# Kernel tuning notes

Hardware: AMD Instinct MI355X
Metric: run time of the kernel (lower is better)

The kernel has to match this reference:

```python
import jax, jax.numpy as jnp
import numpy as np

# SPU activation from the RIAI project: x^2-0.5 for x>=0, sigmoid(-x)-1 for x<0

def _spu(x):
    return jnp.where(x >= 0, x * x - 0.5, jax.nn.sigmoid(-x) - 1.0)

def _spu_grad(x):
    return jnp.where(x <= -50.0, 0.0,
                     jnp.where(x >= 0.0, 2.0 * x, -0.5 / (jnp.cosh(x) + 1.0)))

def _spu_tangent(x0):
    a = _spu_grad(x0)
    return a, _spu(x0) - a * x0

def _tangent_param(l, u, t):
    return _spu_tangent(l * (1.0 - t) + u * t)

def _spu_shifted_over_x(x):
    normal = (x <= -1e-5) | (x > 0)
    safe_x = jnp.where(normal, x, 1.0)  # avoid 0/0 in masked-out lanes
    return jnp.where(normal, (_spu(x) + 0.5) / safe_x, -0.25)

def _binsearch_acceptable_range(l, u):
    req = _spu(u)
    bl, br = l, jnp.zeros_like(l)
    for _ in range(20):  # fixed 20 bisection steps, fully vectorized
        c = 0.5 * (bl + br)
        a, b = _spu_tangent(c)
        covers = a * u + b >= req
        bl = jnp.where(covers, c, bl)
        br = jnp.where(covers, br, c)
    return bl

def _spu_bounds(l, u, tl, tu):
    # endpoint (secant) line through (l,spu(l)) and (u,spu(u))
    yl, yu = _spu(l), _spu(u)
    ea = (yu - yl) / (u - l + 1e-8)
    eb = yl - l * ea

    negative = u <= 0
    positive = l >= 0
    crossing = ~(negative | positive)

    # negative branch (args masked: negative*l, negative*u)
    ln, un = jnp.where(negative, l, 0.0), jnp.where(negative, u, 0.0)
    na, nb = _tangent_param(ln, un, tu)
    # positive branch
    lp, up = jnp.where(positive, l, 0.0), jnp.where(positive, u, 0.0)
    pa, pb = _tangent_param(lp, up, tl)

    # crossing branch: l full, u masked (matches spu_crossing(l, crossing*u))
    uc = jnp.where(crossing, u, 0.0)
    u_end = _binsearch_acceptable_range(l, uc)
    ua, ub_ = _tangent_param(l, u_end, tu)
    not_cov = ua * uc + ub_ <= _spu(uc)
    cr_uw = jnp.where(not_cov, ea, ua)
    cr_ub = jnp.where(not_cov, eb, ub_)
    # bottom tangent (lower bound for crossing)
    den = uc - l
    threshold = -l / jnp.where(den == 0, 1.0, den)
    is_normal = tl >= threshold
    nla, nlb = _tangent_param(l, uc, tl)
    steep = _spu_shifted_over_x(l)
    safe_thr = jnp.where(threshold == 0, 1.0, threshold)
    wa = steep * (1.0 - (tl / safe_thr) ** 2)
    wb = jnp.full_like(nlb, -0.5)
    cr_lw = jnp.where(is_normal, nla, wa)
    cr_lb = jnp.where(is_normal, nlb, wb)

    def comb(n_, p_, c_):
        return (jnp.where(negative, n_, 0.0) + jnp.where(positive, p_, 0.0)
                + jnp.where(crossing, c_, 0.0))

    lw = comb(ea, pa, cr_lw)
    lb = comb(eb, pb, cr_lb)
    uw = comb(na, ea, cr_uw)
    ub = comb(nb, eb, cr_ub)
    return lw, lb, uw, ub

def _substitute(x, yp, yn):
    # pos/neg split + batched matmul; x: (bs,m,n+1), yp/yn: (bs,n,k)
    px = jnp.where(x > 0, x, 0.0)
    nx = jnp.where(x <= 0, x, 0.0)
    new = px[:, :, 1:] @ yp + nx[:, :, 1:] @ yn
    return new.at[:, :, 0].add(x[:, :, 0])

def _forward(l, u, tl_raw, tu_raw):
    bs, n = l.shape
    tl = jax.nn.sigmoid(4.0 * tl_raw)
    tu = jax.nn.sigmoid(4.0 * tu_raw)
    lw, lb, uw, ub = _spu_bounds(l, u, tl, tu)
    idx = jnp.arange(n)
    nal = jnp.zeros((bs, n, n + 1), l.dtype).at[:, idx, idx + 1].set(lw).at[:, :, 0].set(lb)
    nau = jnp.zeros((bs, n, n + 1), l.dtype).at[:, idx, idx + 1].set(uw).at[:, :, 0].set(ub)
    # backsubstitute into the input layer (prev.al = l, prev.au = u as constants)
    al = _substitute(nal, l[:, :, None], u[:, :, None])   # (bs,n,1)
    au = _substitute(nau, u[:, :, None], l[:, :, None])
    return jnp.stack([al[:, :, 0], au[:, :, 0]], axis=-1)  # (bs,n,2) = (nl,nu)

def setup_inputs() -> dict:
    key = jax.random.key(0)
    k1, k2, k3, k4 = jax.random.split(key, 4)
    bs, n = 64, 1024
    center = jax.random.normal(k1, (bs, n), dtype=jnp.float32)
    half = jax.random.uniform(k2, (bs, n), minval=0.05, maxval=2.0, dtype=jnp.float32)
    l = center - half
    u = center + half  # guarantees l < u
    tl_raw = 0.5 * jax.random.normal(k3, (bs, n), dtype=jnp.float32)
    tu_raw = 0.5 * jax.random.normal(k4, (bs, n), dtype=jnp.float32)
    return {"l": l, "u": u, "tl_raw": tl_raw, "tu_raw": tu_raw}

def reference(l, u, tl_raw, tu_raw):
    return _forward(l, u, tl_raw, tu_raw)
```

## Files before the change

kernel.cpp:

```cpp
#include <hip/hip_runtime.h>


__device__ __forceinline__ float frcp(float x) { return __builtin_amdgcn_rcpf(x); }

__device__ __forceinline__ float spu_fast(float x) {
    if (x >= 0.0f) return x * x - 0.5f;
    float t = __expf(x);
    return -t * frcp(1.0f + t);
}

__device__ __forceinline__ float spu_grad_fast(float x) {
    if (x >= 0.0f) return 2.0f * x;
    float t = __expf(x);
    float inv = frcp(1.0f + t);
    return -t * inv * inv;
}

__global__ void __launch_bounds__(256)
spu_bounds_kernel(const float* __restrict__ lp, const float* __restrict__ up,
                  const float* __restrict__ tlr, const float* __restrict__ tur,
                  float2* __restrict__ out, int n) {
    int i = blockIdx.x * blockDim.x + threadIdx.x;
    if (i >= n) return;

    float l  = lp[i];
    float u  = up[i];
    float tl = frcp(1.0f + __expf(-4.0f * tlr[i]));
    float tu = frcp(1.0f + __expf(-4.0f * tur[i]));

    float yl = spu_fast(l), yu = spu_fast(u);
    float ea = (yu - yl) * frcp(u - l + 1e-8f);
    float eb = yl - l * ea;

    float lw, lb, uw, ub;

    if (u <= 0.0f) {
        lw = ea; lb = eb;
        float c = l * (1.0f - tu) + u * tu;
        float a = spu_grad_fast(c);
        uw = a;
        ub = spu_fast(c) - a * c;
    } else if (l >= 0.0f) {
        float c = l * (1.0f - tl) + u * tl;
        float a = 2.0f * c;
        lw = a;
        lb = (c * c - 0.5f) - a * c;
        uw = ea; ub = eb;
    } else {
        float req = u * u - 0.5f;
        float bl = l, br = 0.0f;
        #pragma unroll
        for (int it = 0; it < 20; ++it) {
            float c   = 0.5f * (bl + br);
            float t   = __expf(c);
            float inv = frcp(1.0f + t);
            float s   = -t * inv;
            float a   = s * inv;
            float b   = fmaf(-a, c, s);
            bool covers = fmaf(a, u, b) >= req;
            bl = covers ? c : bl;
            br = covers ? br : c;
        }
        float c2  = l * (1.0f - tu) + bl * tu;
        float t2  = __expf(c2);
        float iv2 = frcp(1.0f + t2);
        float s2  = -t2 * iv2;
        float ua  = s2 * iv2;
        float ub_ = fmaf(-ua, c2, s2);
        bool not_cov = fmaf(ua, u, ub_) <= req;
        uw = not_cov ? ea : ua;
        ub = not_cov ? eb : ub_;

        float den = u - l;
        float threshold = -l * frcp(den);
        if (tl >= threshold) {
            float cl = l * (1.0f - tl) + u * tl;
            float a2 = spu_grad_fast(cl);
            lw = a2;
            lb = spu_fast(cl) - a2 * cl;
        } else {
            bool nrm = (l <= -1e-5f) || (l > 0.0f);
            float steep = nrm ? (spu_fast(l) + 0.5f) * frcp(l) : -0.25f;
            float r = tl * frcp(threshold);
            lw = steep * (1.0f - r * r);
            lb = -0.5f;
        }
    }

    float al = fmaxf(lw, 0.0f) * l + fminf(lw, 0.0f) * u + lb;
    float au = fmaxf(uw, 0.0f) * u + fminf(uw, 0.0f) * l + ub;
    out[i] = make_float2(al, au);
}

extern "C" void kernel_launch(void* const* d_in, const int* in_sizes, int n_in,
                              void* d_out, int out_size, void* d_ws, size_t ws_size,
                              hipStream_t stream) {
    const float* l   = (const float*)d_in[0];
    const float* u   = (const float*)d_in[1];
    const float* tlr = (const float*)d_in[2];
    const float* tur = (const float*)d_in[3];
    float2* out = (float2*)d_out;
    int n = in_sizes[0];
    int block = 256;
    int grid = (n + block - 1) / block;
    spu_bounds_kernel<<<grid, block, 0, stream>>>(l, u, tlr, tur, out, n);
}
```

Baseline: 60.65 us.

## Make SPU bounds branchless and shorten bisection with rcp-free covers test

Replaces the per-case branches with computing all three branches unconditionally and selecting results, which removes wavefront divergence. The bisection is rewritten as a step-halving search whose covers test is multiplied through by (1+e^c)^2, so it needs no reciprocal. Its iteration count drops from 20 to 12. Every lane now does the crossing-branch work, and the fewer iterations may change results slightly near the tolerance.

```diff
diff --git a/kernel.cpp b/kernel.cpp
--- a/kernel.cpp
+++ b/kernel.cpp
@@ -2,19 +2,6 @@
 
 
 __device__ __forceinline__ float frcp(float x) { return __builtin_amdgcn_rcpf(x); }
-
-__device__ __forceinline__ float spu_fast(float x) {
-    if (x >= 0.0f) return x * x - 0.5f;
-    float t = __expf(x);
-    return -t * frcp(1.0f + t);
-}
-
-__device__ __forceinline__ float spu_grad_fast(float x) {
-    if (x >= 0.0f) return 2.0f * x;
-    float t = __expf(x);
-    float inv = frcp(1.0f + t);
-    return -t * inv * inv;
-}
 
 __global__ void __launch_bounds__(256)
 spu_bounds_kernel(const float* __restrict__ lp, const float* __restrict__ up,
@@ -28,64 +15,84 @@
     float tl = frcp(1.0f + __expf(-4.0f * tlr[i]));
     float tu = frcp(1.0f + __expf(-4.0f * tur[i]));
 
-    float yl = spu_fast(l), yu = spu_fast(u);
-    float ea = (yu - yl) * frcp(u - l + 1e-8f);
-    float eb = yl - l * ea;
+    float tL  = __expf(l);
+    float ivL = frcp(1.0f + tL);
+    float yl  = (l >= 0.0f) ? fmaf(l, l, -0.5f) : (-tL * ivL);
+    float tU  = __expf(u);
+    float ivU = frcp(1.0f + tU);
+    float yu  = (u >= 0.0f) ? fmaf(u, u, -0.5f) : (-tU * ivU);
 
-    float lw, lb, uw, ub;
+    float den = u - l;
+    float ea  = (yu - yl) * frcp(den + 1e-8f);
+    float eb  = yl - l * ea;
 
-    if (u <= 0.0f) {
-        lw = ea; lb = eb;
-        float c = l * (1.0f - tu) + u * tu;
-        float a = spu_grad_fast(c);
-        uw = a;
-        ub = spu_fast(c) - a * c;
-    } else if (l >= 0.0f) {
-        float c = l * (1.0f - tl) + u * tl;
-        float a = 2.0f * c;
-        lw = a;
-        lb = (c * c - 0.5f) - a * c;
-        uw = ea; ub = eb;
-    } else {
-        float req = u * u - 0.5f;
-        float bl = l, br = 0.0f;
-        #pragma unroll
-        for (int it = 0; it < 20; ++it) {
-            float c   = 0.5f * (bl + br);
-            float t   = __expf(c);
-            float inv = frcp(1.0f + t);
-            float s   = -t * inv;
-            float a   = s * inv;
-            float b   = fmaf(-a, c, s);
-            bool covers = fmaf(a, u, b) >= req;
-            bl = covers ? c : bl;
-            br = covers ? br : c;
-        }
-        float c2  = l * (1.0f - tu) + bl * tu;
-        float t2  = __expf(c2);
-        float iv2 = frcp(1.0f + t2);
-        float s2  = -t2 * iv2;
-        float ua  = s2 * iv2;
-        float ub_ = fmaf(-ua, c2, s2);
-        bool not_cov = fmaf(ua, u, ub_) <= req;
-        uw = not_cov ? ea : ua;
-        ub = not_cov ? eb : ub_;
+    float cn  = fmaf(den, tu, l);
+    float tn  = __expf(cn);
+    float ivn = frcp(1.0f + tn);
+    float sn  = -tn * ivn;
+    float an  = sn * ivn;
+    float bn  = fmaf(-an, cn, sn);
 
-        float den = u - l;
-        float threshold = -l * frcp(den);
-        if (tl >= threshold) {
-            float cl = l * (1.0f - tl) + u * tl;
-            float a2 = spu_grad_fast(cl);
-            lw = a2;
-            lb = spu_fast(cl) - a2 * cl;
-        } else {
-            bool nrm = (l <= -1e-5f) || (l > 0.0f);
-            float steep = nrm ? (spu_fast(l) + 0.5f) * frcp(l) : -0.25f;
-            float r = tl * frcp(threshold);
-            lw = steep * (1.0f - r * r);
-            lb = -0.5f;
-        }
+    float cp = fmaf(den, tl, l);
+    float pa = 2.0f * cp;
+    float pb = fmaf(-cp, cp, -0.5f);
+
+    float req = fmaf(u, u, -0.5f);
+    float u1  = u + 1.0f;
+
+    float w  = -l;
+    float c  = 0.5f * l;
+    float st = 0.25f * w;
+    float bl = l;
+    #pragma unroll
+    for (int it = 0; it < 12; ++it) {
+        float cmu = c - u1;
+        float cup = c + st;
+        float cdn = c - st;
+        float t   = __expf(c);
+        float q   = 1.0f + t;
+        float lhs = t * (cmu - t);
+        float rhs = req * q * q;
+        bool covers = lhs >= rhs;
+        bl = covers ? c : bl;
+        c  = covers ? cup : cdn;
+        st *= 0.5f;
     }
+
+    float c2  = fmaf(bl - l, tu, l);
+    float t2  = __expf(c2);
+    float iv2 = frcp(1.0f + t2);
+    float s2  = -t2 * iv2;
+    float ua  = s2 * iv2;
+    float ub_ = fmaf(-ua, c2, s2);
+    bool not_cov = fmaf(ua, u, ub_) <= req;
+    float cuw = not_cov ? ea : ua;
+    float cub = not_cov ? eb : ub_;
+
+    float thr = -l * frcp(den);
+    float cl  = fmaf(den, tl, l);
+    float t3  = __expf(cl);
+    float iv3 = frcp(1.0f + t3);
+    float s3  = -t3 * iv3;
+    float a3n = s3 * iv3;
+    float a3  = (cl >= 0.0f) ? 2.0f * cl : a3n;
+    float y3  = (cl >= 0.0f) ? fmaf(cl, cl, -0.5f) : s3;
+    float nla = a3;
+    float nlb = fmaf(-a3, cl, y3);
+    bool  nrm_l = (l <= -1e-5f) || (l > 0.0f);
+    float steep = nrm_l ? (yl + 0.5f) * frcp(l) : -0.25f;
+    float r   = tl * frcp(thr);
+    float wa  = steep * (1.0f - r * r);
+    bool  isn = tl >= thr;
+    float clw = isn ? nla : wa;
+    float clb = isn ? nlb : -0.5f;
+
+    bool neg = (u <= 0.0f);
+    bool pos = (l >= 0.0f);
+    float lw = neg ? ea : (pos ? pa : clw);
+    float lb = neg ? eb : (pos ? pb : clb);
+    float uw = neg ? an : (pos ? ea : cuw);
+    float ub = neg ? bn : (pos ? eb : cub);
 
     float al = fmaxf(lw, 0.0f) * l + fminf(lw, 0.0f) * u + lb;
     float au = fmaxf(uw, 0.0f) * u + fminf(uw, 0.0f) * l + ub;
```

After: 59.17 us. 1.03x faster.
